# Kernel tuning notes

Hardware: AMD Instinct MI355X
Metric: run time of the kernel (lower is better)

Reference implementation:

```python
import jax, jax.numpy as jnp
import numpy as np

N, D, K = 65536, 512, 5


def setup_inputs() -> dict:
    key = jax.random.key(0)
    k0, k1, k2, k3, k4 = jax.random.split(key, 5)
    x = jax.random.normal(k0, (N, D), dtype=jnp.float32)
    is_protected = jax.random.randint(k1, (N,), 0, 2) > 0  # bool mask
    alpha_p = jax.random.uniform(k2, (D,), dtype=jnp.float32, minval=0.9, maxval=1.1)
    classif_w = jax.random.normal(k3, (K, 1), dtype=jnp.float32)
    centroids = jax.random.normal(k4, (K, D), dtype=jnp.float32)
    return {"x": x, "is_protected": is_protected, "alpha_p": alpha_p,
            "classif_w": classif_w, "centroids": centroids}


def reference(x, is_protected, alpha_p, classif_w, centroids):
    # NOTE: original torch forward applies alpha_p to both the protected and
    # non-protected rows (alpha_np is unused), so the mask split is a no-op
    # and we compute the mapping over all rows at once.
    # distances: sum_d alpha_d * (x_nd - c_kd)^2  -> (n, k)
    diff2 = (x[:, None, :] - centroids[None, :, :]) ** 2  # (n, k, d)
    dist = jnp.einsum("nkd,d->nk", diff2, alpha_p)
    mapping = jax.nn.softmax(dist, axis=-1)              # (n, k)
    reconstructed = mapping @ centroids                  # (n, d)
    pred = (mapping @ jax.nn.sigmoid(classif_w)).ravel() # (n,)
    return mapping, reconstructed, pred
```

## Files before the change

### kernel.cpp

```cpp
#include <hip/hip_runtime.h>
#include <math.h>

#define LFR_N 65536
#define LFR_D 512
#define LFR_K 5
#define ROWS  4

__global__ __launch_bounds__(256) void lfr_kernel(
    const float* __restrict__ x,
    const float* __restrict__ alpha,
    const float* __restrict__ w,
    const float* __restrict__ cent,
    float* __restrict__ out_map,
    float* __restrict__ out_rec,
    float* __restrict__ out_pred)
{
    const int lane          = threadIdx.x & 63;
    const int wave_in_block = threadIdx.x >> 6;
    const int wave_id       = blockIdx.x * (blockDim.x >> 6) + wave_in_block;
    const int rb            = wave_id * ROWS;
    if (rb >= LFR_N) return;

    const int d0 = lane * 8;

    float4 xl[ROWS][2];
    #pragma unroll
    for (int r = 0; r < ROWS; ++r) {
        const float* xr = x + (size_t)(rb + r) * LFR_D + d0;
        xl[r][0] = *(const float4*)(xr);
        xl[r][1] = *(const float4*)(xr + 4);
    }

    float al[8];
    {
        float4 a0 = *(const float4*)(alpha + d0);
        float4 a1 = *(const float4*)(alpha + d0 + 4);
        al[0]=a0.x; al[1]=a0.y; al[2]=a0.z; al[3]=a0.w;
        al[4]=a1.x; al[5]=a1.y; al[6]=a1.z; al[7]=a1.w;
    }
    float c[LFR_K][8];
    #pragma unroll
    for (int k = 0; k < LFR_K; ++k) {
        float4 c0 = *(const float4*)(cent + k * LFR_D + d0);
        float4 c1 = *(const float4*)(cent + k * LFR_D + d0 + 4);
        c[k][0]=c0.x; c[k][1]=c0.y; c[k][2]=c0.z; c[k][3]=c0.w;
        c[k][4]=c1.x; c[k][5]=c1.y; c[k][6]=c1.z; c[k][7]=c1.w;
    }
    float sigw[LFR_K];
    #pragma unroll
    for (int k = 0; k < LFR_K; ++k)
        sigw[k] = 1.0f / (1.0f + __expf(-w[k]));

    float xv[ROWS][8];
    #pragma unroll
    for (int r = 0; r < ROWS; ++r) {
        xv[r][0]=xl[r][0].x; xv[r][1]=xl[r][0].y; xv[r][2]=xl[r][0].z; xv[r][3]=xl[r][0].w;
        xv[r][4]=xl[r][1].x; xv[r][5]=xl[r][1].y; xv[r][6]=xl[r][1].z; xv[r][7]=xl[r][1].w;
    }
    float dist[ROWS][LFR_K];
    #pragma unroll
    for (int r = 0; r < ROWS; ++r) {
        #pragma unroll
        for (int k = 0; k < LFR_K; ++k) {
            float acc = 0.0f;
            #pragma unroll
            for (int j = 0; j < 8; ++j) {
                float df = xv[r][j] - c[k][j];
                acc = fmaf(al[j] * df, df, acc);
            }
            dist[r][k] = acc;
        }
    }

    #pragma unroll
    for (int off = 32; off > 0; off >>= 1) {
        #pragma unroll
        for (int r = 0; r < ROWS; ++r)
            #pragma unroll
            for (int k = 0; k < LFR_K; ++k)
                dist[r][k] += __shfl_xor(dist[r][k], off);
    }

    float m[ROWS][LFR_K];
    #pragma unroll
    for (int r = 0; r < ROWS; ++r) {
        float mx = dist[r][0];
        #pragma unroll
        for (int k = 1; k < LFR_K; ++k) mx = fmaxf(mx, dist[r][k]);
        float s = 0.0f;
        #pragma unroll
        for (int k = 0; k < LFR_K; ++k) { m[r][k] = __expf(dist[r][k] - mx); s += m[r][k]; }
        float inv = 1.0f / s;
        #pragma unroll
        for (int k = 0; k < LFR_K; ++k) m[r][k] *= inv;
    }

    #pragma unroll
    for (int r = 0; r < ROWS; ++r) {
        float rv[8];
        #pragma unroll
        for (int j = 0; j < 8; ++j) {
            float acc = m[r][0] * c[0][j];
            #pragma unroll
            for (int k = 1; k < LFR_K; ++k) acc = fmaf(m[r][k], c[k][j], acc);
            rv[j] = acc;
        }
        float* rr = out_rec + (size_t)(rb + r) * LFR_D + d0;
        *(float4*)(rr)     = make_float4(rv[0], rv[1], rv[2], rv[3]);
        *(float4*)(rr + 4) = make_float4(rv[4], rv[5], rv[6], rv[7]);
    }

    #pragma unroll
    for (int r = 0; r < ROWS; ++r) {
        if (lane == r) {
            float* mp = out_map + (size_t)(rb + r) * LFR_K;
            *(float4*)(mp) = make_float4(m[r][0], m[r][1], m[r][2], m[r][3]);
            mp[4] = m[r][4];
            float p = m[r][0] * sigw[0];
            #pragma unroll
            for (int k = 1; k < LFR_K; ++k) p = fmaf(m[r][k], sigw[k], p);
            out_pred[rb + r] = p;
        }
    }
}

extern "C" void kernel_launch(void* const* d_in, const int* in_sizes, int n_in,
                              void* d_out, int out_size, void* d_ws, size_t ws_size,
                              hipStream_t stream) {
    const float* x     = (const float*)d_in[0];
    const float* alpha = (const float*)d_in[2];
    const float* w     = (const float*)d_in[3];
    const float* cent  = (const float*)d_in[4];

    float* out   = (float*)d_out;
    float* o_map = out;
    float* o_rec = out + (size_t)LFR_N * LFR_K;
    float* o_prd = out + (size_t)LFR_N * LFR_K + (size_t)LFR_N * LFR_D;

    dim3 grid(LFR_N / (4 * ROWS)), block(256);
    lfr_kernel<<<grid, block, 0, stream>>>(x, alpha, w, cent, o_map, o_rec, o_prd);
}
```

Measured before the change: 242.3 us.

## Expand distance algebraically, use transpose-style shuffle reduction and nontemporal stores

```diff
diff --git a/kernel.cpp b/kernel.cpp
--- a/kernel.cpp
+++ b/kernel.cpp
@@ -5,6 +5,8 @@
 #define LFR_D 512
 #define LFR_K 5
 #define ROWS  4
+
+typedef float fx4 __attribute__((ext_vector_type(4)));
 
 __global__ __launch_bounds__(256) void lfr_kernel(
     const float* __restrict__ x,
@@ -21,7 +23,9 @@
     const int rb            = wave_id * ROWS;
     if (rb >= LFR_N) return;
 
-    const int d0 = lane * 8;
+    const int d0  = lane * 8;
+    const int hi  = (lane >> 5) & 1;
+    const int mid = (lane >> 4) & 1;
 
     float4 xl[ROWS][2];
     #pragma unroll
@@ -46,10 +50,20 @@
         c[k][0]=c0.x; c[k][1]=c0.y; c[k][2]=c0.z; c[k][3]=c0.w;
         c[k][4]=c1.x; c[k][5]=c1.y; c[k][6]=c1.z; c[k][7]=c1.w;
     }
-    float sigw[LFR_K];
+    float m2a[8];
     #pragma unroll
-    for (int k = 0; k < LFR_K; ++k)
-        sigw[k] = 1.0f / (1.0f + __expf(-w[k]));
+    for (int j = 0; j < 8; ++j) m2a[j] = -2.0f * al[j];
+    float cst[LFR_K];
+    #pragma unroll
+    for (int k = 0; k < LFR_K; ++k) {
+        float s = 0.0f;
+        #pragma unroll
+        for (int j = 0; j < 8; ++j) {
+            float u = al[j] * c[k][j];
+            s = fmaf(u, c[k][j], s);
+        }
+        cst[k] = s;
+    }
 
     float xv[ROWS][8];
     #pragma unroll
@@ -57,42 +71,89 @@
         xv[r][0]=xl[r][0].x; xv[r][1]=xl[r][0].y; xv[r][2]=xl[r][0].z; xv[r][3]=xl[r][0].w;
         xv[r][4]=xl[r][1].x; xv[r][5]=xl[r][1].y; xv[r][6]=xl[r][1].z; xv[r][7]=xl[r][1].w;
     }
-    float dist[ROWS][LFR_K];
+    float p[ROWS][LFR_K];
     #pragma unroll
     for (int r = 0; r < ROWS; ++r) {
+        float v[8];
+        #pragma unroll
+        for (int j = 0; j < 8; ++j) v[j] = m2a[j] * xv[r][j];
         #pragma unroll
         for (int k = 0; k < LFR_K; ++k) {
-            float acc = 0.0f;
+            float acc = cst[k];
             #pragma unroll
-            for (int j = 0; j < 8; ++j) {
-                float df = xv[r][j] - c[k][j];
-                acc = fmaf(al[j] * df, df, acc);
-            }
-            dist[r][k] = acc;
+            for (int j = 0; j < 8; ++j) acc = fmaf(c[k][j], v[j], acc);
+            p[r][k] = acc;
         }
     }
 
+    float q[2][LFR_K];
     #pragma unroll
-    for (int off = 32; off > 0; off >>= 1) {
+    for (int r2 = 0; r2 < 2; ++r2) {
         #pragma unroll
-        for (int r = 0; r < ROWS; ++r)
-            #pragma unroll
-            for (int k = 0; k < LFR_K; ++k)
-                dist[r][k] += __shfl_xor(dist[r][k], off);
+        for (int k = 0; k < LFR_K; ++k) {
+            float send = hi ? p[r2][k]     : p[2 + r2][k];
+            float keep = hi ? p[2 + r2][k] : p[r2][k];
+            q[r2][k] = keep + __shfl_xor(send, 32);
+        }
+    }
+    float s[LFR_K];
+    #pragma unroll
+    for (int k = 0; k < LFR_K; ++k) {
+        float send = mid ? q[0][k] : q[1][k];
+        float keep = mid ? q[1][k] : q[0][k];
+        s[k] = keep + __shfl_xor(send, 16);
+    }
+    #pragma unroll
+    for (int off = 8; off > 0; off >>= 1) {
+        #pragma unroll
+        for (int k = 0; k < LFR_K; ++k)
+            s[k] += __shfl_xor(s[k], off);
     }
 
-    float m[ROWS][LFR_K];
+    float e[LFR_K];
+    {
+        float mx = s[0];
+        #pragma unroll
+        for (int k = 1; k < LFR_K; ++k) mx = fmaxf(mx, s[k]);
+        float sum = 0.0f;
+        #pragma unroll
+        for (int k = 0; k < LFR_K; ++k) { e[k] = __expf(s[k] - mx); sum += e[k]; }
+        float inv = 1.0f / sum;
+        #pragma unroll
+        for (int k = 0; k < LFR_K; ++k) e[k] *= inv;
+    }
+
+    if ((lane & 15) == 0) {
+        const int g = lane >> 4;
+        float sigw[LFR_K];
+        #pragma unroll
+        for (int k = 0; k < LFR_K; ++k)
+            sigw[k] = 1.0f / (1.0f + __expf(-w[k]));
+        float* mp = out_map + (size_t)(rb + g) * LFR_K;
+        *(float4*)(mp) = make_float4(e[0], e[1], e[2], e[3]);
+        mp[4] = e[4];
+        float pr = e[0] * sigw[0];
+        #pragma unroll
+        for (int k = 1; k < LFR_K; ++k) pr = fmaf(e[k], sigw[k], pr);
+        out_pred[rb + g] = pr;
+    }
+
+    float mA[2][LFR_K];
     #pragma unroll
-    for (int r = 0; r < ROWS; ++r) {
-        float mx = dist[r][0];
+    for (int k = 0; k < LFR_K; ++k) {
+        float o = __shfl_xor(e[k], 16);
+        mA[0][k] = mid ? o    : e[k];
+        mA[1][k] = mid ? e[k] : o;
+    }
+    float M[ROWS][LFR_K];
+    #pragma unroll
+    for (int r2 = 0; r2 < 2; ++r2) {
         #pragma unroll
-        for (int k = 1; k < LFR_K; ++k) mx = fmaxf(mx, dist[r][k]);
-        float s = 0.0f;
-        #pragma unroll
-        for (int k = 0; k < LFR_K; ++k) { m[r][k] = __expf(dist[r][k] - mx); s += m[r][k]; }
-        float inv = 1.0f / s;
-        #pragma unroll
-        for (int k = 0; k < LFR_K; ++k) m[r][k] *= inv;
+        for (int k = 0; k < LFR_K; ++k) {
+            float o = __shfl_xor(mA[r2][k], 32);
+            M[r2][k]     = hi ? o         : mA[r2][k];
+            M[2 + r2][k] = hi ? mA[r2][k] : o;
+        }
     }
 
     #pragma unroll
@@ -100,27 +161,16 @@
         float rv[8];
         #pragma unroll
         for (int j = 0; j < 8; ++j) {
-            float acc = m[r][0] * c[0][j];
+            float acc = M[r][0] * c[0][j];
             #pragma unroll
-            for (int k = 1; k < LFR_K; ++k) acc = fmaf(m[r][k], c[k][j], acc);
+            for (int k = 1; k < LFR_K; ++k) acc = fmaf(M[r][k], c[k][j], acc);
             rv[j] = acc;
         }
         float* rr = out_rec + (size_t)(rb + r) * LFR_D + d0;
-        *(float4*)(rr)     = make_float4(rv[0], rv[1], rv[2], rv[3]);
-        *(float4*)(rr + 4) = make_float4(rv[4], rv[5], rv[6], rv[7]);
-    }
-
-    #pragma unroll
-    for (int r = 0; r < ROWS; ++r) {
-        if (lane == r) {
-            float* mp = out_map + (size_t)(rb + r) * LFR_K;
-            *(float4*)(mp) = make_float4(m[r][0], m[r][1], m[r][2], m[r][3]);
-            mp[4] = m[r][4];
-            float p = m[r][0] * sigw[0];
-            #pragma unroll
-            for (int k = 1; k < LFR_K; ++k) p = fmaf(m[r][k], sigw[k], p);
-            out_pred[rb + r] = p;
-        }
+        fx4 v0 = { rv[0], rv[1], rv[2], rv[3] };
+        fx4 v1 = { rv[4], rv[5], rv[6], rv[7] };
+        __builtin_nontemporal_store(v0, (fx4*)(rr));
+        __builtin_nontemporal_store(v1, (fx4*)(rr + 4));
     }
 }
 
```

Measured after the change: 244.4 us. About the same (+0.8%).

## Stage x through swizzled LDS transpose, one row per 4 lanes, 16 rows per wave

Applied to the files above, without the earlier changes.

```diff
diff --git a/kernel.cpp b/kernel.cpp
--- a/kernel.cpp
+++ b/kernel.cpp
@@ -4,7 +4,14 @@
 #define LFR_N 65536
 #define LFR_D 512
 #define LFR_K 5
-#define ROWS  4
+#define RPW   16
+#define WPB   4
+#define NCH   (LFR_D / 64)
+#define BLOCKS (LFR_N / (RPW * WPB))
+
+
+#define LGKM0() do { asm volatile("s_waitcnt lgkmcnt(0)" ::: "memory"); \
+                     __builtin_amdgcn_sched_barrier(0); } while (0)
 
 __global__ __launch_bounds__(256) void lfr_kernel(
     const float* __restrict__ x,
@@ -15,111 +22,126 @@
     float* __restrict__ out_rec,
     float* __restrict__ out_pred)
 {
-    const int lane          = threadIdx.x & 63;
-    const int wave_in_block = threadIdx.x >> 6;
-    const int wave_id       = blockIdx.x * (blockDim.x >> 6) + wave_in_block;
-    const int rb            = wave_id * ROWS;
-    if (rb >= LFR_N) return;
+    __shared__ float  sc[LFR_K][LFR_D];
+    __shared__ float  sa[LFR_D];
+    __shared__ float4 sx[WPB][16][16];
 
-    const int d0 = lane * 8;
+    const int tid  = threadIdx.x;
+    const int lane = tid & 63;
+    const int wib  = tid >> 6;
+    const int rr   = lane & 15;
+    const int qq   = lane >> 4;
 
-    float4 xl[ROWS][2];
-    #pragma unroll
-    for (int r = 0; r < ROWS; ++r) {
-        const float* xr = x + (size_t)(rb + r) * LFR_D + d0;
-        xl[r][0] = *(const float4*)(xr);
-        xl[r][1] = *(const float4*)(xr + 4);
-    }
-
-    float al[8];
     {
-        float4 a0 = *(const float4*)(alpha + d0);
-        float4 a1 = *(const float4*)(alpha + d0 + 4);
-        al[0]=a0.x; al[1]=a0.y; al[2]=a0.z; al[3]=a0.w;
-        al[4]=a1.x; al[5]=a1.y; al[6]=a1.z; al[7]=a1.w;
-    }
-    float c[LFR_K][8];
-    #pragma unroll
-    for (int k = 0; k < LFR_K; ++k) {
-        float4 c0 = *(const float4*)(cent + k * LFR_D + d0);
-        float4 c1 = *(const float4*)(cent + k * LFR_D + d0 + 4);
-        c[k][0]=c0.x; c[k][1]=c0.y; c[k][2]=c0.z; c[k][3]=c0.w;
-        c[k][4]=c1.x; c[k][5]=c1.y; c[k][6]=c1.z; c[k][7]=c1.w;
+        const float4* csrc = (const float4*)cent;
+        float4* cdst = (float4*)&sc[0][0];
+        #pragma unroll
+        for (int i = 0; i < 3; ++i) {
+            int idx = tid + i * 256;
+            if (idx < (LFR_K * LFR_D) / 4) cdst[idx] = csrc[idx];
+        }
+        if (tid < LFR_D / 4) ((float4*)sa)[tid] = ((const float4*)alpha)[tid];
     }
     float sigw[LFR_K];
     #pragma unroll
-    for (int k = 0; k < LFR_K; ++k)
-        sigw[k] = 1.0f / (1.0f + __expf(-w[k]));
+    for (int k = 0; k < LFR_K; ++k) sigw[k] = 1.0f / (1.0f + __expf(-w[k]));
+    __syncthreads();
 
-    float xv[ROWS][8];
+    const int r0 = (blockIdx.x * WPB + wib) * RPW;
+
+    float4 pf[4];
     #pragma unroll
-    for (int r = 0; r < ROWS; ++r) {
-        xv[r][0]=xl[r][0].x; xv[r][1]=xl[r][0].y; xv[r][2]=xl[r][0].z; xv[r][3]=xl[r][0].w;
-        xv[r][4]=xl[r][1].x; xv[r][5]=xl[r][1].y; xv[r][6]=xl[r][1].z; xv[r][7]=xl[r][1].w;
-    }
-    float dist[ROWS][LFR_K];
+    for (int i = 0; i < 4; ++i)
+        pf[i] = *(const float4*)(x + (size_t)(r0 + i*4 + qq) * LFR_D + rr*4);
+
+    float dacc[LFR_K] = {0.f, 0.f, 0.f, 0.f, 0.f};
+
     #pragma unroll
-    for (int r = 0; r < ROWS; ++r) {
+    for (int ch = 0; ch < NCH; ++ch) {
+        if (ch) LGKM0();
         #pragma unroll
-        for (int k = 0; k < LFR_K; ++k) {
-            float acc = 0.0f;
+        for (int i = 0; i < 4; ++i) {
+            const int row = i*4 + qq;
+            sx[wib][row][rr ^ row] = pf[i];
+        }
+        if (ch + 1 < NCH) {
             #pragma unroll
-            for (int j = 0; j < 8; ++j) {
-                float df = xv[r][j] - c[k][j];
-                acc = fmaf(al[j] * df, df, acc);
+            for (int i = 0; i < 4; ++i)
+                pf[i] = *(const float4*)(x + (size_t)(r0 + i*4 + qq) * LFR_D
+                                           + (ch + 1) * 64 + rr*4);
+        }
+        LGKM0();
+        #pragma unroll
+        for (int j4 = 0; j4 < 4; ++j4) {
+            const int col4 = qq*4 + j4;
+            float4 xv = sx[wib][rr][col4 ^ rr];
+            float4 av = ((const float4*)&sa[ch * 64])[col4];
+            #pragma unroll
+            for (int k = 0; k < LFR_K; ++k) {
+                float4 cv = ((const float4*)&sc[k][ch * 64])[col4];
+                float d0 = xv.x - cv.x, d1 = xv.y - cv.y;
+                float d2 = xv.z - cv.z, d3 = xv.w - cv.w;
+                dacc[k] = fmaf(av.x * d0, d0, dacc[k]);
+                dacc[k] = fmaf(av.y * d1, d1, dacc[k]);
+                dacc[k] = fmaf(av.z * d2, d2, dacc[k]);
+                dacc[k] = fmaf(av.w * d3, d3, dacc[k]);
             }
-            dist[r][k] = acc;
         }
     }
 
     #pragma unroll
-    for (int off = 32; off > 0; off >>= 1) {
-        #pragma unroll
-        for (int r = 0; r < ROWS; ++r)
-            #pragma unroll
-            for (int k = 0; k < LFR_K; ++k)
-                dist[r][k] += __shfl_xor(dist[r][k], off);
+    for (int k = 0; k < LFR_K; ++k) {
+        dacc[k] += __shfl_xor(dacc[k], 16);
+        dacc[k] += __shfl_xor(dacc[k], 32);
     }
 
-    float m[ROWS][LFR_K];
+    float e[LFR_K];
+    float mx = dacc[0];
     #pragma unroll
-    for (int r = 0; r < ROWS; ++r) {
-        float mx = dist[r][0];
+    for (int k = 1; k < LFR_K; ++k) mx = fmaxf(mx, dacc[k]);
+    float sum = 0.f;
+    #pragma unroll
+    for (int k = 0; k < LFR_K; ++k) { e[k] = __expf(dacc[k] - mx); sum += e[k]; }
+    float inv = 1.0f / sum;
+    #pragma unroll
+    for (int k = 0; k < LFR_K; ++k) e[k] *= inv;
+
+    if (qq == 0) {
+        float* mp = out_map + (size_t)(r0 + rr) * LFR_K;
         #pragma unroll
-        for (int k = 1; k < LFR_K; ++k) mx = fmaxf(mx, dist[r][k]);
-        float s = 0.0f;
+        for (int k = 0; k < LFR_K; ++k) mp[k] = e[k];
+        float pr = e[0] * sigw[0];
         #pragma unroll
-        for (int k = 0; k < LFR_K; ++k) { m[r][k] = __expf(dist[r][k] - mx); s += m[r][k]; }
-        float inv = 1.0f / s;
-        #pragma unroll
-        for (int k = 0; k < LFR_K; ++k) m[r][k] *= inv;
+        for (int k = 1; k < LFR_K; ++k) pr = fmaf(e[k], sigw[k], pr);
+        out_pred[r0 + rr] = pr;
     }
 
     #pragma unroll
-    for (int r = 0; r < ROWS; ++r) {
-        float rv[8];
+    for (int ch = 0; ch < NCH; ++ch) {
+        LGKM0();
         #pragma unroll
-        for (int j = 0; j < 8; ++j) {
-            float acc = m[r][0] * c[0][j];
+        for (int j4 = 0; j4 < 4; ++j4) {
+            const int col4 = qq*4 + j4;
+            float4 c0 = ((const float4*)&sc[0][ch * 64])[col4];
+            float4 rv;
+            rv.x = e[0] * c0.x; rv.y = e[0] * c0.y;
+            rv.z = e[0] * c0.z; rv.w = e[0] * c0.w;
             #pragma unroll
-            for (int k = 1; k < LFR_K; ++k) acc = fmaf(m[r][k], c[k][j], acc);
-            rv[j] = acc;
+            for (int k = 1; k < LFR_K; ++k) {
+                float4 cv = ((const float4*)&sc[k][ch * 64])[col4];
+                rv.x = fmaf(e[k], cv.x, rv.x);
+                rv.y = fmaf(e[k], cv.y, rv.y);
+                rv.z = fmaf(e[k], cv.z, rv.z);
+                rv.w = fmaf(e[k], cv.w, rv.w);
+            }
+            sx[wib][rr][col4 ^ rr] = rv;
         }
-        float* rr = out_rec + (size_t)(rb + r) * LFR_D + d0;
-        *(float4*)(rr)     = make_float4(rv[0], rv[1], rv[2], rv[3]);
-        *(float4*)(rr + 4) = make_float4(rv[4], rv[5], rv[6], rv[7]);
-    }
-
-    #pragma unroll
-    for (int r = 0; r < ROWS; ++r) {
-        if (lane == r) {
-            float* mp = out_map + (size_t)(rb + r) * LFR_K;
-            *(float4*)(mp) = make_float4(m[r][0], m[r][1], m[r][2], m[r][3]);
-            mp[4] = m[r][4];
-            float p = m[r][0] * sigw[0];
-            #pragma unroll
-            for (int k = 1; k < LFR_K; ++k) p = fmaf(m[r][k], sigw[k], p);
-            out_pred[rb + r] = p;
+        LGKM0();
+        #pragma unroll
+        for (int i = 0; i < 4; ++i) {
+            const int row = i*4 + qq;
+            float4 v = sx[wib][row][rr ^ row];
+            *(float4*)(out_rec + (size_t)(r0 + row) * LFR_D + ch * 64 + rr*4) = v;
         }
     }
 }
@@ -137,6 +159,6 @@
     float* o_rec = out + (size_t)LFR_N * LFR_K;
     float* o_prd = out + (size_t)LFR_N * LFR_K + (size_t)LFR_N * LFR_D;
 
-    dim3 grid(LFR_N / (4 * ROWS)), block(256);
+    dim3 grid(BLOCKS), block(256);
     lfr_kernel<<<grid, block, 0, stream>>>(x, alpha, w, cent, o_map, o_rec, o_prd);
 }
```

Measured after the change: 248.0 us. +2.4%, slower.
